# Kernel optimization log

Measured on AMD Instinct MI355X. Metric: run time of the kernel, lower is better.

## Reference

```python
import jax, jax.numpy as jnp
import numpy as np
from jax import lax

Q = 8          # num quantization bins (co_matrix_shape[0])
K = 3          # spatial filter size (spatial_shape = [K,K,K])
PAD = (K - 1) // 2


def setup_inputs() -> dict:
    key = jax.random.key(0)
    k1, k2, k3 = jax.random.split(key, 3)
    # uniform [0,1) so floor((x-min)/max * Q) stays in [0, Q-1] (matches valid torch index_select)
    x = jax.random.uniform(k1, (8, 16, 256, 256), dtype=jnp.float32)
    co_matrix = jax.random.normal(k2, (Q, Q), dtype=jnp.float32)
    spatial_filter = jax.random.normal(k3, (K, K, K), dtype=jnp.float32)
    return {"input": x, "co_matrix": co_matrix, "spatial_filter": spatial_filter}


def _quantize(x, num_q):
    # faithful to the torch code: norm = (x - min) / max  (NOT max-min)
    x_min = jnp.min(x)
    x_max = jnp.max(x)
    idx = jnp.floor((x - x_min) / x_max * num_q).astype(jnp.int32)  # [N,c,h,w]
    return idx


def reference(input, co_matrix, spatial_filter):
    x = input
    N, c, h, w = x.shape
    idx = _quantize(x, Q)                                  # [N,c,h,w] int32

    # Vectorize the per-bin loop: gather row i of co_matrix at every pixel's bin index.
    # cof[i] = co_matrix[i, idx]  -> [Q,N,c,h,w]
    cof = co_matrix[:, idx]
    conv_in = (cof * x[None]).reshape(Q * N, 1, c, h, w)   # [Q*N,1,c,h,w]

    w3d = spatial_filter.reshape(1, 1, K, K, K)
    spatial = lax.conv_general_dilated(
        conv_in, w3d,
        window_strides=(1, 1, 1),
        padding=[(PAD, PAD)] * 3,
        dimension_numbers=("NCDHW", "OIDHW", "NCDHW"),
    ).reshape(Q, N, c, h, w)

    # torch code convolves the mask with a 1x1x1 ones filter at stride 1 -> identity
    mask = (idx[None] == jnp.arange(Q, dtype=jnp.int32)[:, None, None, None, None])
    conv_out = jnp.sum(mask.astype(x.dtype) * spatial, axis=0)  # [N,c,h,w]
    return (conv_out, co_matrix, spatial_filter, idx)
```

## Files before the change

kernel.cpp:

```cpp
#include <hip/hip_runtime.h>
#include <stdint.h>

__device__ __forceinline__ uint32_t mapf(float f) {
  uint32_t u = __float_as_uint(f);
  return (u & 0x80000000u) ? ~u : (u | 0x80000000u);
}
__device__ __forceinline__ float unmapf(uint32_t m) {
  return (m & 0x80000000u) ? __uint_as_float(m & 0x7FFFFFFFu) : __uint_as_float(~m);
}


__global__ __launch_bounds__(256) void k_minmax(const float* __restrict__ x, int n4, int ntail,
                                                const float* __restrict__ co, const float* __restrict__ sfil,
                                                uint32_t* __restrict__ wsu,
                                                float* __restrict__ out_co, float* __restrict__ out_sf) {
  __shared__ float smn[256], smx[256];
  int tid = threadIdx.x;
  float mn = 3.0e38f, mx = -3.0e38f;
  const float4* x4 = (const float4*)x;
  int stride = gridDim.x * blockDim.x;
  #pragma unroll 4
  for (int i = blockIdx.x * blockDim.x + tid; i < n4; i += stride) {
    float4 v = x4[i];
    mn = fminf(mn, fminf(fminf(v.x, v.y), fminf(v.z, v.w)));
    mx = fmaxf(mx, fmaxf(fmaxf(v.x, v.y), fmaxf(v.z, v.w)));
  }
  if (blockIdx.x == 0 && tid == 0) {
    for (int i = 4 * n4; i < 4 * n4 + ntail; ++i) { mn = fminf(mn, x[i]); mx = fmaxf(mx, x[i]); }
  }
  smn[tid] = mn; smx[tid] = mx;
  __syncthreads();
  for (int s = 128; s > 0; s >>= 1) {
    if (tid < s) { smn[tid] = fminf(smn[tid], smn[tid + s]); smx[tid] = fmaxf(smx[tid], smx[tid + s]); }
    __syncthreads();
  }
  if (tid == 0) {
    int slot = blockIdx.x & 15;
    atomicMax(&wsu[64 + slot], mapf(smx[0]));
    atomicMax(&wsu[80 + slot], mapf(-smn[0]));
  }
  if (blockIdx.x == 0) {
    if (tid < 8) {
      const float* r = co + tid * 8;
      float rmn = r[0], rmx = r[0];
      #pragma unroll
      for (int j = 1; j < 8; ++j) { rmn = fminf(rmn, r[j]); rmx = fmaxf(rmx, r[j]); }
      float rs = (rmx - rmn) * (1.0f / 255.0f);
      if (rs < 1e-30f) rs = 1.0f;
      uint32_t d0 = 0, d1 = 0;
      #pragma unroll
      for (int j = 0; j < 8; ++j) {
        int b = (int)lrintf((r[j] - rmn) / rs);
        b = b < 0 ? 0 : (b > 255 ? 255 : b);
        if (j < 4) d0 |= ((uint32_t)b) << (8 * j);
        else       d1 |= ((uint32_t)b) << (8 * (j - 4));
      }
      wsu[8 + 4 * tid + 0] = d0;
      wsu[8 + 4 * tid + 1] = d1;
      wsu[8 + 4 * tid + 2] = __float_as_uint(rs);
      wsu[8 + 4 * tid + 3] = __float_as_uint(rmn);
    }
    if (tid < 64) out_co[tid] = co[tid];
    if (tid < 27) out_sf[tid] = sfil[tid];
  }
}

__device__ __forceinline__ float quant_d8(float xv, float mn, float mx8, float y8) {
  float s   = xv - mn;
  float t08 = s * y8;
  float r0  = __builtin_fmaf(-mx8, t08, s);
  return __builtin_fmaf(r0, y8, t08);
}

__global__ __launch_bounds__(256) void k_conv(const float* __restrict__ x, const float* __restrict__ sfil,
                                              const uint32_t* __restrict__ wsu,
                                              float* __restrict__ out, float* __restrict__ out_idx) {
  __shared__ __align__(16) float    xs[5280];
  __shared__ __align__(16) uint32_t qls[1320];
  __shared__ __align__(16) uint4    tbl[8];

  int tid = threadIdx.x;
  int b = blockIdx.x;
  int wt = b & 1, ht = (b >> 1) & 31, ct = (b >> 6) & 7, n = b >> 9;
  int c0 = ct * 2, h0 = ht * 8, w0 = wt * 128;
  int nbase = n * 16;

  if (tid < 8) tbl[tid] = ((const uint4*)(wsu + 8))[tid];

  uint32_t ma = 0u, mb = 0u;
  #pragma unroll
  for (int i = 0; i < 16; ++i) {
    uint32_t a = wsu[64 + i], bq = wsu[80 + i];
    ma = ma > a ? ma : a;
    mb = mb > bq ? mb : bq;
  }
  float mx = unmapf(ma);
  float mn = -unmapf(mb);
  float y   = 1.0f / mx;
  float y8  = y * 8.0f;
  float mx8 = mx * 0.125f;

  const int tx = tid & 31, ty = tid >> 5;

  {
    const int xoff = 4 * tx;
    #pragma unroll
    for (int it = 0; it < 5; ++it) {
      int rr = ty + 8 * it;
      int lc = (rr * 13) >> 7;
      int lh = rr - 10 * lc;
      int c = c0 - 1 + lc, h = h0 - 1 + lh;
      bool chok = ((unsigned)c < 16u) & ((unsigned)h < 256u);
      int chbase = ((nbase + c) << 16) + (h << 8);
      int wq = w0 + 4 * tx;
      float4 vb = float4{0.f, 0.f, 0.f, 0.f};
      if (chok) vb = *(const float4*)&x[chbase + wq];
      float pe = __shfl_up(vb.w, 1);
      if (tx == 0) {
        int wm = wq - 1;
        pe = (chok & (wm >= 0)) ? x[chbase + wm] : 0.0f;
      }
      float xv[4] = {pe, vb.x, vb.y, vb.z};
      uint32_t qu[4];
      #pragma unroll
      for (int j = 0; j < 4; ++j) {
        int q = (int)quant_d8(xv[j], mn, mx8, y8);
        qu[j] = min((uint32_t)q, 7u);
      }
      uint32_t b01 = __builtin_amdgcn_perm(qu[1], qu[0], 0x0c0c0400u);
      uint32_t b23 = __builtin_amdgcn_perm(qu[3], qu[2], 0x04000c0cu);
      *(float4*)&xs[rr * 132 + xoff] = float4{xv[0], xv[1], xv[2], xv[3]};
      qls[rr * 33 + tx] = b01 | b23;
    }
    if (tid < 40) {
      int rr = tid;
      int lc = (rr * 13) >> 7;
      int lh = rr - 10 * lc;
      int c = c0 - 1 + lc, h = h0 - 1 + lh;
      bool chok = ((unsigned)c < 16u) & ((unsigned)h < 256u);
      int chbase = ((nbase + c) << 16) + (h << 8);
      int wq = w0 + 128;
      float4 vb = float4{0.f, 0.f, 0.f, 0.f};
      if (chok & (wq < 256)) vb = *(const float4*)&x[chbase + wq];
      float pe = chok ? x[chbase + wq - 1] : 0.0f;
      float xv[4] = {pe, vb.x, vb.y, vb.z};
      uint32_t qu[4];
      #pragma unroll
      for (int j = 0; j < 4; ++j) {
        int q = (int)quant_d8(xv[j], mn, mx8, y8);
        qu[j] = min((uint32_t)q, 7u);
      }
      uint32_t b01 = __builtin_amdgcn_perm(qu[1], qu[0], 0x0c0c0400u);
      uint32_t b23 = __builtin_amdgcn_perm(qu[3], qu[2], 0x04000c0cu);
      *(float4*)&xs[rr * 132 + 128] = float4{xv[0], xv[1], xv[2], xv[3]};
      qls[rr * 33 + 32] = b01 | b23;
    }
  }
  __syncthreads();

  float wf[27];
  #pragma unroll
  for (int i = 0; i < 27; ++i) wf[i] = sfil[i];

  const int tw = tx, th = ty;
  const uint32_t SELK[4] = {0x03020100u, 0x04030201u, 0x05040302u, 0x06050403u};

  for (int c = 0; c < 2; ++c) {
    int xbase = (c * 10 + th) * 132 + 4 * tw;
    int qbase = (c * 10 + th) * 33 + tw;

    int qc = qbase + 11 * 33;
    uint32_t Qc0 = qls[qc], Qc1 = qls[qc + 1];
    uint32_t q4 = __builtin_amdgcn_perm(Qc1, Qc0, 0x04030201u);
    uint32_t rlo[4], rhi[4]; float rs4[4], rc4[4];
    #pragma unroll
    for (int k = 0; k < 4; ++k) {
      uint32_t qk = (q4 >> (8 * k)) & 0xffu;
      uint4 T = tbl[qk];
      rlo[k] = T.x; rhi[k] = T.y;
      rs4[k] = __uint_as_float(T.z); rc4[k] = __uint_as_float(T.w);
    }

    float acc1[4] = {0.f, 0.f, 0.f, 0.f};
    float acc2[4] = {0.f, 0.f, 0.f, 0.f};
    float4 cxA; float2 cxB;
    #pragma unroll
    for (int dc = 0; dc < 3; ++dc) {
      #pragma unroll
      for (int di = 0; di < 3; ++di) {
        int xo = xbase + (dc * 10 + di) * 132;
        float4 A = *(const float4*)&xs[xo];
        float2 B = *(const float2*)&xs[xo + 4];
        if (dc == 1 && di == 1) { cxA = A; cxB = B; }
        int qo = qbase + (dc * 10 + di) * 33;
        uint32_t Q0 = qls[qo], Q1 = qls[qo + 1];
        float xw[6] = {A.x, A.y, A.z, A.w, B.x, B.y};
        const float* wr = &wf[dc * 9 + di * 3];
        #pragma unroll
        for (int k = 0; k < 4; ++k) {
          uint32_t sel = __builtin_amdgcn_perm(Q1, Q0, SELK[k]);
          uint32_t bb  = __builtin_amdgcn_perm(rhi[k], rlo[k], sel);
          float b0 = (float)(bb & 0xffu);
          float b1 = (float)((bb >> 8) & 0xffu);
          float b2 = (float)((bb >> 16) & 0xffu);
          float p0 = wr[0] * xw[k];
          float p1 = wr[1] * xw[k + 1];
          float p2 = wr[2] * xw[k + 2];
          acc2[k] += p0 + p1 + p2;
          acc1[k] = __builtin_fmaf(p0, b0, acc1[k]);
          acc1[k] = __builtin_fmaf(p1, b1, acc1[k]);
          acc1[k] = __builtin_fmaf(p2, b2, acc1[k]);
        }
      }
    }

    float cx[4] = {cxA.y, cxA.z, cxA.w, cxB.x};
    float idxf[4]; float vals[4];
    #pragma unroll
    for (int k = 0; k < 4; ++k) {
      float d8 = quant_d8(cx[k], mn, mx8, y8);
      idxf[k] = truncf(d8);
      float v = __builtin_fmaf(rs4[k], acc1[k], rc4[k] * acc2[k]);
      vals[k] = (d8 >= 8.0f) ? 0.0f : v;
    }

    int gbase = ((nbase + c0 + c) << 16) + ((h0 + th) << 8) + (w0 + 4 * tw);
    *(float4*)&out[gbase] = float4{vals[0], vals[1], vals[2], vals[3]};
    out_idx[gbase + 0] = idxf[0];
    *(float2*)&out_idx[gbase + 1] = float2{idxf[1], idxf[2]};
    out_idx[gbase + 3] = idxf[3];
  }
}

extern "C" void kernel_launch(void* const* d_in, const int* in_sizes, int n_in,
                              void* d_out, int out_size, void* d_ws, size_t ws_size,
                              hipStream_t stream) {
  const float* x    = (const float*)d_in[0];
  const float* co   = (const float*)d_in[1];
  const float* sfil = (const float*)d_in[2];
  float* out = (float*)d_out;
  uint32_t* wsu = (uint32_t*)d_ws;
  int nx = in_sizes[0];

  int n4 = nx / 4, ntail = nx - 4 * n4;

  float* out_co  = out + nx;
  float* out_sf  = out + nx + 64;
  float* out_idx = out + nx + 64 + 27;

  hipMemsetAsync(wsu + 64, 0, 128, stream);

  k_minmax<<<512, 256, 0, stream>>>(x, n4, ntail, co, sfil, wsu, out_co, out_sf);
  k_conv<<<4096, 256, 0, stream>>>(x, sfil, wsu, out, out_idx);
}
```

Measured before the change: 134.4 us.

## Stage input tile in fp16 and accumulate with packed dot2 instructions

Stores the shared-memory input tile as packed fp16 and packs the filter weights to fp16. The 3x3x3 stencil then runs with packed half multiplies and v_dot2_f32_f16 accumulation, which halves LDS footprint and traffic and cuts ALU instruction count. The co-matrix bytes become fp16 operands through a 1024-bias trick, corrected in the per-bin constant. The fp32 reload of the centre pixel now happens only when some tile has an out-of-range bin. The minmax grid is raised and an occupancy hint is added. The trade-off is fp16 rounding of inputs, weights and products, which may exceed tolerance.

```diff
diff --git a/kernel.cpp b/kernel.cpp
--- a/kernel.cpp
+++ b/kernel.cpp
@@ -1,5 +1,7 @@
 #include <hip/hip_runtime.h>
 #include <stdint.h>
+
+typedef __fp16 h2 __attribute__((ext_vector_type(2)));
 
 __device__ __forceinline__ uint32_t mapf(float f) {
   uint32_t u = __float_as_uint(f);
@@ -7,6 +9,16 @@
 }
 __device__ __forceinline__ float unmapf(uint32_t m) {
   return (m & 0x80000000u) ? __uint_as_float(m & 0x7FFFFFFFu) : __uint_as_float(~m);
+}
+
+__device__ __forceinline__ float fdot2f(h2 a, h2 b, float c) {
+#if __has_builtin(__builtin_amdgcn_fdot2)
+  return __builtin_amdgcn_fdot2(a, b, c, false);
+#else
+  float d;
+  asm("v_dot2_f32_f16 %0, %1, %2, %3" : "=v"(d) : "v"(a), "v"(b), "v"(c));
+  return d;
+#endif
 }
 
 
@@ -72,12 +84,13 @@
   return __builtin_fmaf(r0, y8, t08);
 }
 
-__global__ __launch_bounds__(256) void k_conv(const float* __restrict__ x, const float* __restrict__ sfil,
+__global__ __launch_bounds__(256, 8) void k_conv(const float* __restrict__ x, const float* __restrict__ sfil,
                                               const uint32_t* __restrict__ wsu,
                                               float* __restrict__ out, float* __restrict__ out_idx) {
-  __shared__ __align__(16) float    xs[5280];
+  __shared__ __align__(16) uint32_t xsu[2640];
   __shared__ __align__(16) uint32_t qls[1320];
   __shared__ __align__(16) uint4    tbl[8];
+  __shared__ uint32_t anyw[4];
 
   int tid = threadIdx.x;
   int b = blockIdx.x;
@@ -101,9 +114,9 @@
   float mx8 = mx * 0.125f;
 
   const int tx = tid & 31, ty = tid >> 5;
+  int qmaxv = 0;
 
   {
-    const int xoff = 4 * tx;
     #pragma unroll
     for (int it = 0; it < 5; ++it) {
       int rr = ty + 8 * it;
@@ -125,11 +138,15 @@
       #pragma unroll
       for (int j = 0; j < 4; ++j) {
         int q = (int)quant_d8(xv[j], mn, mx8, y8);
+        qmaxv = max(qmaxv, q);
         qu[j] = min((uint32_t)q, 7u);
       }
       uint32_t b01 = __builtin_amdgcn_perm(qu[1], qu[0], 0x0c0c0400u);
       uint32_t b23 = __builtin_amdgcn_perm(qu[3], qu[2], 0x04000c0cu);
-      *(float4*)&xs[rr * 132 + xoff] = float4{xv[0], xv[1], xv[2], xv[3]};
+      h2 lo = __builtin_amdgcn_cvt_pkrtz(xv[0], xv[1]);
+      h2 hi = __builtin_amdgcn_cvt_pkrtz(xv[2], xv[3]);
+      uint2 wv; wv.x = __builtin_bit_cast(uint32_t, lo); wv.y = __builtin_bit_cast(uint32_t, hi);
+      *(uint2*)&xsu[rr * 66 + 2 * tx] = wv;
       qls[rr * 33 + tx] = b01 | b23;
     }
     if (tid < 40) {
@@ -148,83 +165,107 @@
       #pragma unroll
       for (int j = 0; j < 4; ++j) {
         int q = (int)quant_d8(xv[j], mn, mx8, y8);
+        qmaxv = max(qmaxv, q);
         qu[j] = min((uint32_t)q, 7u);
       }
       uint32_t b01 = __builtin_amdgcn_perm(qu[1], qu[0], 0x0c0c0400u);
       uint32_t b23 = __builtin_amdgcn_perm(qu[3], qu[2], 0x04000c0cu);
-      *(float4*)&xs[rr * 132 + 128] = float4{xv[0], xv[1], xv[2], xv[3]};
+      h2 lo = __builtin_amdgcn_cvt_pkrtz(xv[0], xv[1]);
+      h2 hi = __builtin_amdgcn_cvt_pkrtz(xv[2], xv[3]);
+      uint2 wv; wv.x = __builtin_bit_cast(uint32_t, lo); wv.y = __builtin_bit_cast(uint32_t, hi);
+      *(uint2*)&xsu[rr * 66 + 64] = wv;
       qls[rr * 33 + 32] = b01 | b23;
     }
   }
+  anyw[tid >> 6] = (uint32_t)__any(qmaxv > 7);
   __syncthreads();
-
-  float wf[27];
+  uint32_t any8 = anyw[0] | anyw[1] | anyw[2] | anyw[3];
+
+  uint32_t wAs[9], wBs[9];
   #pragma unroll
-  for (int i = 0; i < 27; ++i) wf[i] = sfil[i];
-
+  for (int r = 0; r < 9; ++r) {
+    h2 a  = __builtin_amdgcn_cvt_pkrtz(sfil[3 * r], sfil[3 * r + 1]);
+    h2 bq = __builtin_amdgcn_cvt_pkrtz(sfil[3 * r + 2], 0.0f);
+    wAs[r] = (uint32_t)__builtin_amdgcn_readfirstlane((int)__builtin_bit_cast(uint32_t, a));
+    wBs[r] = (uint32_t)__builtin_amdgcn_readfirstlane((int)__builtin_bit_cast(uint32_t, bq));
+  }
+
+  const h2 one2 = {(__fp16)1.0f, (__fp16)1.0f};
+  const uint32_t SELK[4] = {0x03020100u, 0x04030201u, 0x05040302u, 0x06050403u};
   const int tw = tx, th = ty;
-  const uint32_t SELK[4] = {0x03020100u, 0x04030201u, 0x05040302u, 0x06050403u};
 
   for (int c = 0; c < 2; ++c) {
-    int xbase = (c * 10 + th) * 132 + 4 * tw;
     int qbase = (c * 10 + th) * 33 + tw;
+    int xbase = (c * 10 + th) * 66 + 2 * tw;
 
     int qc = qbase + 11 * 33;
     uint32_t Qc0 = qls[qc], Qc1 = qls[qc + 1];
     uint32_t q4 = __builtin_amdgcn_perm(Qc1, Qc0, 0x04030201u);
-    uint32_t rlo[4], rhi[4]; float rs4[4], rc4[4];
+    uint32_t rlo[4], rhi[4]; float rs4[4], rcp4[4];
     #pragma unroll
     for (int k = 0; k < 4; ++k) {
       uint32_t qk = (q4 >> (8 * k)) & 0xffu;
       uint4 T = tbl[qk];
       rlo[k] = T.x; rhi[k] = T.y;
-      rs4[k] = __uint_as_float(T.z); rc4[k] = __uint_as_float(T.w);
+      rs4[k] = __uint_as_float(T.z);
+      rcp4[k] = __builtin_fmaf(-1024.0f, rs4[k], __uint_as_float(T.w));
     }
 
     float acc1[4] = {0.f, 0.f, 0.f, 0.f};
     float acc2[4] = {0.f, 0.f, 0.f, 0.f};
-    float4 cxA; float2 cxB;
     #pragma unroll
     for (int dc = 0; dc < 3; ++dc) {
       #pragma unroll
       for (int di = 0; di < 3; ++di) {
-        int xo = xbase + (dc * 10 + di) * 132;
-        float4 A = *(const float4*)&xs[xo];
-        float2 B = *(const float2*)&xs[xo + 4];
-        if (dc == 1 && di == 1) { cxA = A; cxB = B; }
+        int xo = xbase + (dc * 10 + di) * 66;
         int qo = qbase + (dc * 10 + di) * 33;
+        uint2 px = *(const uint2*)&xsu[xo];
+        uint32_t p2u = xsu[xo + 2];
         uint32_t Q0 = qls[qo], Q1 = qls[qo + 1];
-        float xw[6] = {A.x, A.y, A.z, A.w, B.x, B.y};
-        const float* wr = &wf[dc * 9 + di * 3];
+        uint32_t m01 = __builtin_amdgcn_alignbit(px.y, px.x, 16);
+        uint32_t m12 = __builtin_amdgcn_alignbit(p2u, px.y, 16);
+        uint32_t m5  = __builtin_amdgcn_alignbit(p2u, p2u, 16);
+        uint32_t xAu[4] = {px.x, m01, px.y, m12};
+        uint32_t xBu[4] = {px.y, m12, p2u, m5};
+        int r = dc * 3 + di;
+        h2 wA = __builtin_bit_cast(h2, wAs[r]);
+        h2 wB = __builtin_bit_cast(h2, wBs[r]);
         #pragma unroll
         for (int k = 0; k < 4; ++k) {
           uint32_t sel = __builtin_amdgcn_perm(Q1, Q0, SELK[k]);
           uint32_t bb  = __builtin_amdgcn_perm(rhi[k], rlo[k], sel);
-          float b0 = (float)(bb & 0xffu);
-          float b1 = (float)((bb >> 8) & 0xffu);
-          float b2 = (float)((bb >> 16) & 0xffu);
-          float p0 = wr[0] * xw[k];
-          float p1 = wr[1] * xw[k + 1];
-          float p2 = wr[2] * xw[k + 2];
-          acc2[k] += p0 + p1 + p2;
-          acc1[k] = __builtin_fmaf(p0, b0, acc1[k]);
-          acc1[k] = __builtin_fmaf(p1, b1, acc1[k]);
-          acc1[k] = __builtin_fmaf(p2, b2, acc1[k]);
+          uint32_t fA  = __builtin_amdgcn_perm(0x64646464u, bb, 0x04010400u);
+          uint32_t fB  = __builtin_amdgcn_perm(0x64646464u, bb, 0x04040402u);
+          h2 pA = wA * __builtin_bit_cast(h2, xAu[k]);
+          h2 pB = wB * __builtin_bit_cast(h2, xBu[k]);
+          acc1[k] = fdot2f(pA, __builtin_bit_cast(h2, fA), acc1[k]);
+          acc1[k] = fdot2f(pB, __builtin_bit_cast(h2, fB), acc1[k]);
+          acc2[k] = fdot2f(pA, one2, acc2[k]);
+          acc2[k] = fdot2f(pB, one2, acc2[k]);
         }
       }
     }
 
-    float cx[4] = {cxA.y, cxA.z, cxA.w, cxB.x};
-    float idxf[4]; float vals[4];
-    #pragma unroll
-    for (int k = 0; k < 4; ++k) {
-      float d8 = quant_d8(cx[k], mn, mx8, y8);
-      idxf[k] = truncf(d8);
-      float v = __builtin_fmaf(rs4[k], acc1[k], rc4[k] * acc2[k]);
-      vals[k] = (d8 >= 8.0f) ? 0.0f : v;
-    }
-
     int gbase = ((nbase + c0 + c) << 16) + ((h0 + th) << 8) + (w0 + 4 * tw);
+    float idxf[4], vals[4];
+    if (!any8) {
+      #pragma unroll
+      for (int k = 0; k < 4; ++k) {
+        idxf[k] = (float)((q4 >> (8 * k)) & 0xffu);
+        vals[k] = __builtin_fmaf(rs4[k], acc1[k], rcp4[k] * acc2[k]);
+      }
+    } else {
+      float4 cxv = *(const float4*)&x[gbase];
+      float cx[4] = {cxv.x, cxv.y, cxv.z, cxv.w};
+      #pragma unroll
+      for (int k = 0; k < 4; ++k) {
+        float d8 = quant_d8(cx[k], mn, mx8, y8);
+        idxf[k] = truncf(d8);
+        float v = __builtin_fmaf(rs4[k], acc1[k], rcp4[k] * acc2[k]);
+        vals[k] = (d8 >= 8.0f) ? 0.0f : v;
+      }
+    }
+
     *(float4*)&out[gbase] = float4{vals[0], vals[1], vals[2], vals[3]};
     out_idx[gbase + 0] = idxf[0];
     *(float2*)&out_idx[gbase + 1] = float2{idxf[1], idxf[2]};
@@ -250,6 +291,6 @@
 
   hipMemsetAsync(wsu + 64, 0, 128, stream);
 
-  k_minmax<<<512, 256, 0, stream>>>(x, n4, ntail, co, sfil, wsu, out_co, out_sf);
+  k_minmax<<<2048, 256, 0, stream>>>(x, n4, ntail, co, sfil, wsu, out_co, out_sf);
   k_conv<<<4096, 256, 0, stream>>>(x, sfil, wsu, out, out_idx);
 }
```

Result: slower. 147.2 us (+9.5%).
